# Kernel tuning notes

Hardware: AMD Instinct MI355X
Metric: run time of the kernel (lower is better)

## Reference

```python
import jax, jax.numpy as jnp
import numpy as np

B, S = 8, 256
CHAR_V, CHAR_E = 8000, 128
BI_V, BI_E = 200000, 64
EMBED = CHAR_E + 2 * BI_E  # 256
H = 256
NUM_TAGS = 17


def setup_inputs() -> dict:
    key = jax.random.key(0)
    ks = jax.random.split(key, 16)
    s = lambda k, shape, fan: jax.random.normal(k, shape, jnp.float32) * (1.0 / np.sqrt(fan))
    return {
        "tokens": jax.random.randint(ks[0], (B, S, 3), 0, CHAR_V),
        "masks": jnp.ones((B, S), jnp.int32),
        "char_emb": jax.random.normal(ks[1], (CHAR_V, CHAR_E), jnp.float32) * 0.1,
        "bigram_emb": jax.random.normal(ks[2], (BI_V, BI_E), jnp.float32) * 0.1,
        "conv1_w": s(ks[3], (1, EMBED, H), EMBED),
        "conv1_b": jnp.zeros((H,), jnp.float32),
        "conv3_w": s(ks[4], (3, EMBED, H), 3 * EMBED),
        "conv3_b": jnp.zeros((H,), jnp.float32),
        "conv5_w": s(ks[5], (5, EMBED, H), 5 * EMBED),
        "conv5_b": jnp.zeros((H,), jnp.float32),
        "W0": s(ks[6], (H, H), H),
        "b0": jnp.zeros((H,), jnp.float32),
        "W1": s(ks[7], (H, H), H),
        "b1": jnp.zeros((H,), jnp.float32),
        "Wo": s(ks[8], (H, NUM_TAGS), H),
        "bo": jnp.zeros((NUM_TAGS,), jnp.float32),
    }


def _conv_tanh(x, w, b):
    # x: [B,S,E], w: [K,E,H] -> tanh(conv1d same) [B,S,H]
    y = jax.lax.conv_general_dilated(
        x, w, window_strides=(1,), padding="SAME",
        dimension_numbers=("NWC", "WIO", "NWC"))
    return jnp.tanh(y + b)


def _forward(tokens, masks, char_emb, bigram_emb,
             conv1_w, conv1_b, conv3_w, conv3_b, conv5_w, conv5_b,
             W0, b0, W1, b1, Wo, bo):
    # embeddings: char + two bigram lookups -> [B,S,EMBED]
    x = jnp.concatenate([
        char_emb[tokens[:, :, 0]],
        bigram_emb[tokens[:, :, 1]],
        bigram_emb[tokens[:, :, 2]],
    ], axis=-1)
    # ContextLayer: elementwise max over 3 tanh-conv scales
    c = jnp.maximum(_conv_tanh(x, conv1_w, conv1_b),
                    jnp.maximum(_conv_tanh(x, conv3_w, conv3_b),
                                _conv_tanh(x, conv5_w, conv5_b)))  # [B,S,H]
    # RelationLayer: pairwise sigmoid gates, masked mean over j
    m = masks.astype(jnp.float32)                      # [B,S]
    lengths = jnp.sum(m, axis=1)                       # [B]
    g0 = c @ W0 + b0                                   # [B,S,H]
    g1 = c @ W1 + b1                                   # [B,S,H]
    gate = jax.nn.sigmoid(g0[:, :, None, :] + g1[:, None, :, :])  # [B,S,S,H]
    pair_mask = m[:, :, None] * m[:, None, :]          # [B,S,S]
    ctx = jnp.einsum("bij,bijh->bih", pair_mask, gate * c[:, None, :, :])
    ctx = ctx / lengths[:, None, None]
    rel = jnp.tanh(ctx)                                # [B,S,H]
    logits = rel @ Wo + bo                             # [B,S,T]
    return jax.nn.softmax(logits, axis=-1)


def reference(tokens, masks, char_emb, bigram_emb,
              conv1_w, conv1_b, conv3_w, conv3_b, conv5_w, conv5_b,
              W0, b0, W1, b1, Wo, bo):
    return _forward(tokens, masks, char_emb, bigram_emb,
                    conv1_w, conv1_b, conv3_w, conv3_b, conv5_w, conv5_b,
                    W0, b0, W1, b1, Wo, bo)
```

## Files before the change

kernel.cpp:

```cpp
#include <hip/hip_runtime.h>
#include <hip/hip_bf16.h>

#define BB 8
#define SS 256
#define CHAR_E 128
#define BI_E 64
#define EMBED 256
#define HH 256
#define NTAGS 17
#define SPAD 260
#define NROWS 2048
#define NLOG2E -1.4426950408889634f

typedef __attribute__((ext_vector_type(8))) short short8;
typedef __attribute__((ext_vector_type(4))) float f32x4;
typedef __attribute__((ext_vector_type(2))) float f32x2;
#define MFMA16(a, b, c) __builtin_amdgcn_mfma_f32_16x16x32_bf16(a, b, c, 0, 0, 0)

__device__ __forceinline__ float fast_rcp(float x) {
    return __builtin_amdgcn_rcpf(x);
}
__device__ __forceinline__ float fast_exp2(float x) {
    return __builtin_amdgcn_exp2f(x);
}
__device__ __forceinline__ float fast_tanh(float x) {
    float e = __expf(2.0f * x);
    return 1.0f - 2.0f * fast_rcp(e + 1.0f);
}

__global__ __launch_bounds__(256) void embed_pack_kernel(
        const int* __restrict__ tokens,
        const float* __restrict__ char_emb,
        const float* __restrict__ bigram_emb,
        const float* __restrict__ w1, const float* __restrict__ w3,
        const float* __restrict__ w5,
        const float* __restrict__ W0, const float* __restrict__ W1mat,
        const int* __restrict__ masks,
        __hip_bfloat16* __restrict__ xbf,
        __hip_bfloat16* __restrict__ WcombT,
        __hip_bfloat16* __restrict__ W01T,
        float* __restrict__ Linv_buf) {
    int blk = blockIdx.x;
    int t = threadIdx.x;
    if (blk < BB * SPAD) {
        int b = blk / SPAD, r = blk % SPAD;
        float v = 0.0f;
        if (r >= 2 && r < SS + 2) {
            int s = r - 2;
            const int* tk = tokens + (b * SS + s) * 3;
            if (t < CHAR_E)              v = char_emb[tk[0] * CHAR_E + t];
            else if (t < CHAR_E + BI_E)  v = bigram_emb[tk[1] * BI_E + (t - CHAR_E)];
            else                         v = bigram_emb[tk[2] * BI_E + (t - CHAR_E - BI_E)];
        }
        xbf[blk * EMBED + t] = __float2bfloat16(v);
    } else if (blk < BB * SPAD + 160) {
        int kk0 = (blk - BB * SPAD) * 8;
        int h = t, hc = h >> 4, hl = h & 15;
        union { short8 v; __hip_bfloat16 b[8]; } u5, u3, u1;
        #pragma unroll
        for (int k = 0; k < 8; ++k) {
            int kk = kk0 + k, tap = kk >> 8, e = kk & 255;
            float f5 = w5[(tap * EMBED + e) * HH + h];
            float f3 = (tap >= 1 && tap <= 3) ? w3[((tap - 1) * EMBED + e) * HH + h] : 0.f;
            float f1 = (tap == 2) ? w1[e * HH + h] : 0.f;
            u5.b[k] = __float2bfloat16(f5);
            u3.b[k] = __float2bfloat16(f3);
            u1.b[k] = __float2bfloat16(f1);
        }
        *(short8*)(WcombT + (hc * 48 +  0 + hl) * 1280 + kk0) = u5.v;
        *(short8*)(WcombT + (hc * 48 + 16 + hl) * 1280 + kk0) = u3.v;
        *(short8*)(WcombT + (hc * 48 + 32 + hl) * 1280 + kk0) = u1.v;
    } else if (blk < BB * SPAD + 160 + 256) {
        int e = blk - BB * SPAD - 160;
        W01T[t * 256 + e]         = __float2bfloat16(W0[e * HH + t]);
        W01T[(256 + t) * 256 + e] = __float2bfloat16(W1mat[e * HH + t]);
    } else {
        int b = t >> 5, l = t & 31;
        int ssum = 0;
        #pragma unroll
        for (int k = 0; k < 8; ++k) ssum += masks[b * SS + l * 8 + k];
        #pragma unroll
        for (int o = 16; o; o >>= 1) ssum += __shfl_xor(ssum, o);
        if (l == 0) Linv_buf[b] = (ssum > 0) ? (1.0f / (float)ssum) : 0.0f;
    }
}

__global__ __launch_bounds__(256, 2) void conv_mfma_fused(
        const __hip_bfloat16* __restrict__ xbf,
        const __hip_bfloat16* __restrict__ WcombT,
        const float* __restrict__ cb1, const float* __restrict__ cb3,
        const float* __restrict__ cb5,
        const int* __restrict__ masks, const float* __restrict__ Linv_buf,
        __hip_bfloat16* __restrict__ cbf, float* __restrict__ cmT) {
    __shared__ short8 sA[2][1024];
    __shared__ short8 sB[2][768];

    int blk = blockIdx.x;
    int slot = blk >> 3;
    int mt = (blk & 7) * 4 + (slot >> 4);
    int hc = slot & 15;
    int tid = threadIdx.x, w = tid >> 6, lane = tid & 63;
    int fr = lane & 15, fq = lane >> 4;
    int row0 = mt * 64;
    int b = row0 >> 8, s0 = row0 & 255;
    const __hip_bfloat16* xbase = xbf + (b * SPAD + s0) * EMBED;
    const __hip_bfloat16* wbase = WcombT + (hc * 48) * 1280;

    short8 va[4], vb[3];
    auto LOADG = [&](int q) {
        int tap = q >> 1, e0 = (q & 1) * 128;
        const __hip_bfloat16* xs = xbase + tap * EMBED + e0;
        #pragma unroll
        for (int it = 0; it < 4; ++it) {
            int s = tid + it * 256, r = s >> 4, cg = s & 15;
            va[it] = *(const short8*)(xs + r * EMBED + cg * 8);
        }
        const __hip_bfloat16* wsrc = wbase + q * 128;
        #pragma unroll
        for (int it = 0; it < 3; ++it) {
            int s = tid + it * 256, r = s >> 4, cg = s & 15;
            vb[it] = *(const short8*)(wsrc + r * 1280 + cg * 8);
        }
    };
    auto WRITE = [&](int buf) {
        #pragma unroll
        for (int it = 0; it < 4; ++it) {
            int s = tid + it * 256, r = s >> 4, cg = s & 15;
            sA[buf][r * 16 + (cg ^ (r & 15))] = va[it];
        }
        #pragma unroll
        for (int it = 0; it < 3; ++it) {
            int s = tid + it * 256, r = s >> 4, cg = s & 15;
            sB[buf][r * 16 + (cg ^ (r & 15))] = vb[it];
        }
    };

    LOADG(0);
    WRITE(0);
    __syncthreads();

    f32x4 acc0 = {}, acc1 = {}, acc2 = {};
    int ra = w * 16 + fr;
    int cur = 0;
    for (int q = 0; q < 10; ++q) {
        if (q < 9) LOADG(q + 1);
        #pragma unroll
        for (int ks = 0; ks < 4; ++ks) {
            int c = ks * 4 + fq;
            short8 a  = sA[cur][ra * 16 + (c ^ (ra & 15))];
            short8 q0 = sB[cur][fr * 16        + (c ^ fr)];
            short8 q1 = sB[cur][(16 + fr) * 16 + (c ^ fr)];
            short8 q2 = sB[cur][(32 + fr) * 16 + (c ^ fr)];
            acc0 = MFMA16(a, q0, acc0);
            acc1 = MFMA16(a, q1, acc1);
            acc2 = MFMA16(a, q2, acc2);
        }
        if (q < 9) WRITE(cur ^ 1);
        __syncthreads();
        cur ^= 1;
    }

    int h = hc * 16 + fr;
    float bb5 = cb5[h], bb3 = cb3[h], bb1 = cb1[h];
    float Linv = Linv_buf[b];
    #pragma unroll
    for (int j = 0; j < 4; ++j) {
        int row = row0 + w * 16 + fq * 4 + j;
        float t5 = fast_tanh(acc0[j] + bb5);
        float t3 = fast_tanh(acc1[j] + bb3);
        float t1 = fast_tanh(acc2[j] + bb1);
        float v = fmaxf(t1, fmaxf(t3, t5));
        cbf[row * HH + h] = __float2bfloat16(v);
        cmT[h * NROWS + row] = v * (float)masks[row] * Linv;
    }
}

__global__ __launch_bounds__(256) void gemm_g_mfma_kernel(
        const __hip_bfloat16* __restrict__ cbf,
        const __hip_bfloat16* __restrict__ W01T,
        const float* __restrict__ b0, const float* __restrict__ b1v,
        float* __restrict__ E0T, float* __restrict__ E1T) {
    __shared__ float s_out[64][33];

    int blk = blockIdx.x;
    int by = blk >> 3, bx = blk & 7;
    int tid = threadIdx.x;
    int w = tid >> 6, lane = tid & 63;
    int wr = w >> 1, wc = w & 1;
    int m0 = by * 32 + wr * 16;
    int n0 = bx * 64 + wc * 32;
    int fr = lane & 15, fq = lane >> 4;

    const short8* ap  = (const short8*)(cbf + (m0 + fr) * HH + fq * 8);
    const short8* bp0 = (const short8*)(W01T + (n0 + fr) * HH + fq * 8);
    const short8* bp1 = (const short8*)(W01T + (n0 + 16 + fr) * HH + fq * 8);

    short8 af[8], bf0[8], bf1[8];
    #pragma unroll
    for (int ks = 0; ks < 8; ++ks) af[ks] = ap[ks * 4];
    #pragma unroll
    for (int ks = 0; ks < 8; ++ks) { bf0[ks] = bp0[ks * 4]; bf1[ks] = bp1[ks * 4]; }

    f32x4 acc[2] = {};
    #pragma unroll
    for (int ks = 0; ks < 8; ++ks) {
        acc[0] = MFMA16(af[ks], bf0[ks], acc[0]);
        acc[1] = MFMA16(af[ks], bf1[ks], acc[1]);
    }
    #pragma unroll
    for (int n = 0; n < 2; ++n) {
        int col = n0 + n * 16 + fr;
        float bias = (col < 256) ? b0[col] : b1v[col - 256];
        int cl = wc * 32 + n * 16 + fr;
        #pragma unroll
        for (int j = 0; j < 4; ++j) {
            int rl = wr * 16 + fq * 4 + j;
            s_out[cl][rl] = fast_exp2(NLOG2E * (acc[n][j] + bias));
        }
    }
    __syncthreads();
    {
        float* dstbase = (bx < 4) ? (E0T + (bx * 64) * NROWS)
                                  : (E1T + (bx * 64 - 256) * NROWS);
        int cl = tid >> 2, rq = tid & 3;
        f32x4 o0, o1;
        #pragma unroll
        for (int k = 0; k < 4; ++k) { o0[k] = s_out[cl][rq * 8 + k];
                                      o1[k] = s_out[cl][rq * 8 + 4 + k]; }
        float* dst = dstbase + cl * NROWS + by * 32 + rq * 8;
        *(f32x4*)dst = o0;
        *(f32x4*)(dst + 4) = o1;
    }
}

__global__ __launch_bounds__(256) void relation_kernel(
        const float* __restrict__ E0T, const float* __restrict__ E1T,
        const float* __restrict__ cmT, const int* __restrict__ masks,
        float* __restrict__ relT) {
    int blk = blockIdx.x;
    int b = blk >> 8, h = blk & 255;
    int i = threadIdx.x;
    int row = b * SS + i;

    const float* e1p = E1T + h * NROWS + b * SS;
    const float* cmp = cmT + h * NROWS + b * SS;

    float e0 = E0T[h * NROWS + row];
    float acc = 0.f;
    #pragma unroll 8
    for (int j = 0; j < SS; ++j) {
        float e1 = e1p[j];
        float cm = cmp[j];
        acc = fmaf(fast_rcp(fmaf(e0, e1, 1.0f)), cm, acc);
    }
    float mi = (float)masks[row];
    relT[h * NROWS + row] = fast_tanh(acc * mi);
}

__global__ __launch_bounds__(256) void final_kernel(
        const float* __restrict__ relT,
        const float* __restrict__ Wo, const float* __restrict__ bo,
        float* __restrict__ out) {
    int blk = blockIdx.x;
    int b = blk >> 3, iblk = blk & 7;
    int tid = threadIdx.x;
    int hg = tid >> 5, il = tid & 31;
    int row = b * SS + iblk * 32 + il;

    __shared__ float wo_s[HH * NTAGS];
    __shared__ float part[8][32][NTAGS];

    for (int idx = tid; idx < HH * NTAGS; idx += 256) wo_s[idx] = Wo[idx];
    __syncthreads();

    float acc[NTAGS];
    #pragma unroll
    for (int t = 0; t < NTAGS; ++t) acc[t] = 0.f;
    const float* rbase = relT + row;
    for (int k = 0; k < 32; ++k) {
        int hh = hg * 32 + k;
        float v = rbase[hh * NROWS];
        const float* wrow = wo_s + hh * NTAGS;
        #pragma unroll
        for (int t = 0; t < NTAGS; ++t) acc[t] = fmaf(v, wrow[t], acc[t]);
    }
    #pragma unroll
    for (int t = 0; t < NTAGS; ++t) part[hg][il][t] = acc[t];
    __syncthreads();

    for (int idx = tid; idx < 32 * NTAGS; idx += 256) {
        int ii = idx / NTAGS, t = idx - ii * NTAGS;
        float s = bo[t];
        #pragma unroll
        for (int g = 0; g < 8; ++g) s += part[g][ii][t];
        part[0][ii][t] = s;
    }
    __syncthreads();

    if (tid < 32) {
        float mx = -1e30f;
        #pragma unroll
        for (int t = 0; t < NTAGS; ++t) mx = fmaxf(mx, part[0][tid][t]);
        float ex[NTAGS], sum = 0.f;
        #pragma unroll
        for (int t = 0; t < NTAGS; ++t) { ex[t] = __expf(part[0][tid][t] - mx); sum += ex[t]; }
        float si = fast_rcp(sum);
        int orow = b * SS + iblk * 32 + tid;
        #pragma unroll
        for (int t = 0; t < NTAGS; ++t)
            out[orow * NTAGS + t] = ex[t] * si;
    }
}

extern "C" void kernel_launch(void* const* d_in, const int* in_sizes, int n_in,
                              void* d_out, int out_size, void* d_ws, size_t ws_size,
                              hipStream_t stream) {
    const int*   tokens     = (const int*)d_in[0];
    const int*   masks      = (const int*)d_in[1];
    const float* char_emb   = (const float*)d_in[2];
    const float* bigram_emb = (const float*)d_in[3];
    const float* conv1_w    = (const float*)d_in[4];
    const float* conv1_b    = (const float*)d_in[5];
    const float* conv3_w    = (const float*)d_in[6];
    const float* conv3_b    = (const float*)d_in[7];
    const float* conv5_w    = (const float*)d_in[8];
    const float* conv5_b    = (const float*)d_in[9];
    const float* W0         = (const float*)d_in[10];
    const float* b0         = (const float*)d_in[11];
    const float* W1         = (const float*)d_in[12];
    const float* b1         = (const float*)d_in[13];
    const float* Wo         = (const float*)d_in[14];
    const float* bo         = (const float*)d_in[15];
    float* out = (float*)d_out;

    char* p = (char*)d_ws;
    __hip_bfloat16* xbf    = (__hip_bfloat16*)p;  p += BB * SPAD * EMBED * 2;
    __hip_bfloat16* WcombT = (__hip_bfloat16*)p;  p += 768 * 1280 * 2;
    __hip_bfloat16* W01T   = (__hip_bfloat16*)p;  p += 512 * 256 * 2;
    __hip_bfloat16* cbf    = (__hip_bfloat16*)p;  p += NROWS * HH * 2;
    float* cmT  = (float*)p;  p += (size_t)HH * NROWS * 4;
    float* E0T  = (float*)p;  p += (size_t)HH * NROWS * 4;
    float* E1T  = (float*)p;  p += (size_t)HH * NROWS * 4;
    float* relT = (float*)p;  p += (size_t)HH * NROWS * 4;
    float* Linv_buf = (float*)p;  p += 64;

    embed_pack_kernel<<<BB * SPAD + 160 + 256 + 1, 256, 0, stream>>>(
        tokens, char_emb, bigram_emb, conv1_w, conv3_w, conv5_w, W0, W1,
        masks, xbf, WcombT, W01T, Linv_buf);
    conv_mfma_fused<<<512, 256, 0, stream>>>(xbf, WcombT, conv1_b, conv3_b,
                                             conv5_b, masks, Linv_buf, cbf, cmT);
    gemm_g_mfma_kernel<<<512, 256, 0, stream>>>(cbf, W01T, b0, b1, E0T, E1T);
    relation_kernel<<<BB * 256, 256, 0, stream>>>(E0T, E1T, cmT, masks, relT);
    final_kernel<<<BB * 8, 256, 0, stream>>>(relT, Wo, bo, out);
}
```

Before: 63.02 us.

## Broadcast relation-kernel j-values via readlane instead of per-iteration loads

The relation kernel now loads the E1 and cm vectors into registers once per wave and broadcasts each element with readlane. This replaces the per-iteration uniform global/scalar loads inside the 256-step inner loop. The conv kernel's block-to-tile mapping is also simplified to a plain mt/hc split, dropping the previous interleaved swizzle. The readlane loop is fully unrolled, so code size grows, and the mapping change may alter cache locality.

```diff
diff --git a/kernel.cpp b/kernel.cpp
--- a/kernel.cpp
+++ b/kernel.cpp
@@ -26,6 +26,9 @@
 __device__ __forceinline__ float fast_tanh(float x) {
     float e = __expf(2.0f * x);
     return 1.0f - 2.0f * fast_rcp(e + 1.0f);
+}
+__device__ __forceinline__ float readlane_f(float v, int l) {
+    return __int_as_float(__builtin_amdgcn_readlane(__float_as_int(v), l));
 }
 
 __global__ __launch_bounds__(256) void embed_pack_kernel(
@@ -96,9 +99,7 @@
     __shared__ short8 sB[2][768];
 
     int blk = blockIdx.x;
-    int slot = blk >> 3;
-    int mt = (blk & 7) * 4 + (slot >> 4);
-    int hc = slot & 15;
+    int mt = blk >> 4, hc = blk & 15;
     int tid = threadIdx.x, w = tid >> 6, lane = tid & 63;
     int fr = lane & 15, fq = lane >> 4;
     int row0 = mt * 64;
@@ -239,19 +240,28 @@
         float* __restrict__ relT) {
     int blk = blockIdx.x;
     int b = blk >> 8, h = blk & 255;
-    int i = threadIdx.x;
-    int row = b * SS + i;
-
-    const float* e1p = E1T + h * NROWS + b * SS;
-    const float* cmp = cmT + h * NROWS + b * SS;
+    int tid = threadIdx.x;
+    int lane = tid & 63;
+    int base = b * SS;
+    int row = base + tid;
+
+    float e1r[4], cmr[4];
+    #pragma unroll
+    for (int k = 0; k < 4; ++k) {
+        e1r[k] = E1T[h * NROWS + base + k * 64 + lane];
+        cmr[k] = cmT[h * NROWS + base + k * 64 + lane];
+    }
 
     float e0 = E0T[h * NROWS + row];
     float acc = 0.f;
-    #pragma unroll 8
-    for (int j = 0; j < SS; ++j) {
-        float e1 = e1p[j];
-        float cm = cmp[j];
-        acc = fmaf(fast_rcp(fmaf(e0, e1, 1.0f)), cm, acc);
+    #pragma unroll
+    for (int k = 0; k < 4; ++k) {
+        #pragma unroll
+        for (int l = 0; l < 64; ++l) {
+            float e1 = readlane_f(e1r[k], l);
+            float cm = readlane_f(cmr[k], l);
+            acc = fmaf(fast_rcp(fmaf(e0, e1, 1.0f)), cm, acc);
+        }
     }
     float mi = (float)masks[row];
     relT[h * NROWS + row] = fast_tanh(acc * mi);
```

After: 67.07 us. +6.4%, slower.
